# Kernel tuning notes

Measured on AMD Instinct MI355X. Metric: run time of the kernel, lower is better.

The kernel has to match this reference:

```python
import jax, jax.numpy as jnp
import numpy as np

BATCH = 160
INSTANCES = 4
FEAT = 1024
P = BATCH // INSTANCES  # number of identity groups

# sigmas from mmd_loss (original uses float64; fp32 here, tiny sigmas underflow exp to 0 identically)
SIGMAS = np.array([1e-06, 1e-05, 1e-04, 1e-03, 1e-02, 1e-01, 1.0, 5.0, 10.0, 15.0,
                   20.0, 25.0, 30.0, 35.0, 100.0, 1e3, 1e4, 1e5, 1e6], dtype=np.float32)

# replicate the quirky block-pair ordering of the original double loop:
# bct starts with (0,1), then for i in 1..P-1, all j != i.
_PAIRS = [(0, 1)] + [(i, j) for i in range(1, P) for j in range(P) if j != i]
PAIR_I = np.array([p[0] for p in _PAIRS], dtype=np.int32)
PAIR_J = np.array([p[1] for p in _PAIRS], dtype=np.int32)


def _sqdist(a, b):
    # ||a_i - b_j||^2 via matmul identity (same math as euclidean_squared_distance)
    an = jnp.sum(a * a, axis=1)
    bn = jnp.sum(b * b, axis=1)
    return an[:, None] + bn[None, :] - 2.0 * (a @ b.T)


def _gk_mean(x, y):
    # mean over the multi-bandwidth Gaussian kernel matrix: mean(sum_k exp(-d/(2 s_k)))
    d = _sqdist(x, y)
    tot = jnp.float32(0.0)
    for s in SIGMAS:
        tot = tot + jnp.mean(jnp.exp(d * jnp.float32(-1.0 / (2.0 * s))))
    return tot


def _mmd_loss(x, y):
    return _gk_mean(x, x) + _gk_mean(y, y) - 2.0 * _gk_mean(x, y)


def _group_dist_blocks(feats):
    # feats: [BATCH, FEAT] -> all-pairs group distance matrices D[p,q] in [P,P,I,I]
    t = feats.reshape(P, INSTANCES, FEAT)
    tn = jnp.sum(t * t, axis=-1)                      # [P, I]
    cross = jnp.einsum('pif,qjf->pqij', t, t)         # [P, P, I, I]
    D = tn[:, None, :, None] + tn[None, :, None, :] - 2.0 * cross
    wc = D[jnp.arange(P), jnp.arange(P)].reshape(P * INSTANCES, INSTANCES)
    bc = D[PAIR_I, PAIR_J].reshape(-1, INSTANCES)     # [(1+(P-1)^2)*I, I]
    return wc, bc


def setup_inputs() -> dict:
    key = jax.random.key(0)
    k1, k2 = jax.random.split(key)
    return {
        'source_features': jax.random.normal(k1, (BATCH, FEAT), dtype=jnp.float32),
        'target_features': jax.random.normal(k2, (BATCH, FEAT), dtype=jnp.float32),
    }


def reference(source_features, target_features):
    wct, bct = _group_dist_blocks(target_features)
    wcs, bcs = _group_dist_blocks(source_features)
    wcs = jax.lax.stop_gradient(wcs)  # .detach() in original
    bcs = jax.lax.stop_gradient(bcs)
    return (_mmd_loss(wcs, wct), _mmd_loss(bcs, bct))
```

## Files before the change

kernel.cpp:

```cpp
#include <hip/hip_runtime.h>


#define FEAT   1024
#define NROW   160
#define NBC    6088
#define NWC    160
#define NPAD   512

#define WS_ES   0
#define WS_ET   25600
#define WS_BCI  51200
#define WS_WCI  104000
#define WS_TAB  109376
#define WS_ACC_BYTES 460032
#define NSLOT  64

#define TAB_N    2816
#define TAB_BASE 16640

#define GK_BC    6088
#define GK_WCEND 6128
#define GK_GRID  6141

struct Coef { float c[19]; };

#if defined(__has_builtin)
#if __has_builtin(__builtin_amdgcn_exp2f)
#define EXP2(x) __builtin_amdgcn_exp2f(x)
#else
#define EXP2(x) exp2f(x)
#endif
#else
#define EXP2(x) exp2f(x)
#endif

__device__ __forceinline__ float sig13(float d, const Coef& co) {
    float s = 0.f;
    #pragma unroll
    for (int k = 6; k < 19; ++k) s += EXP2(d * co.c[k]);
    return s;
}

__device__ __forceinline__ float sqd(float4 a, float4 b) {
    float d0 = a.x - b.x, d1 = a.y - b.y, d2 = a.z - b.z, d3 = a.w - b.w;
    float d = d0 * d0;
    d = fmaf(d1, d1, d);
    d = fmaf(d2, d2, d);
    return fmaf(d3, d3, d);
}

__global__ __launch_bounds__(256) void compute_E_tab(const float* __restrict__ Fs,
                                                     const float* __restrict__ Ft,
                                                     float* __restrict__ ws, Coef co) {
    int b = blockIdx.x;
    if (b >= 200) {
        int k = (b - 200) * 256 + threadIdx.x;
        unsigned u_lo = (unsigned)(TAB_BASE + k) << 16;
        float d_lo = __uint_as_float(u_lo);
        float d_mi = __uint_as_float(u_lo + 0x8000u);
        float d_hi = __uint_as_float(u_lo + 0x10000u);
        float f_lo = sig13(d_lo, co), f_mi = sig13(d_mi, co), f_hi = sig13(d_hi, co);
        float2 e;
        e.x = f_lo + 0.5f * (f_mi - 0.5f * (f_lo + f_hi));
        e.y = (f_hi - f_lo) * (1.0f / 65536.0f);
        ((float2*)(ws + WS_TAB))[k] = e;
        return;
    }
    int side = b / 100;
    int tile = b % 100;
    int trow = tile / 10, tcol = tile % 10;
    const float* F = side ? Ft : Fs;
    float* E = ws + (side ? WS_ET : WS_ES);

    __shared__ float As[16][132];
    __shared__ float Bs[16][132];
    int tid = threadIdx.x;
    int ti = tid >> 4, tj = tid & 15;
    int lr = tid >> 5;
    int lc4 = tid & 31;

    float acc = 0.f;
    for (int ch = 0; ch < 8; ++ch) {
        for (int rr = lr; rr < 16; rr += 8) {
            float4 a = *(const float4*)(F + (trow*16+rr)*FEAT + ch*128 + lc4*4);
            *(float4*)(&As[rr][lc4*4]) = a;
            float4 bb = *(const float4*)(F + (tcol*16+rr)*FEAT + ch*128 + lc4*4);
            *(float4*)(&Bs[rr][lc4*4]) = bb;
        }
        __syncthreads();
        #pragma unroll
        for (int c = 0; c < 128; c += 4) {
            float4 a = *(const float4*)(&As[ti][c]);
            float4 bb = *(const float4*)(&Bs[tj][c]);
            float d0 = a.x - bb.x, d1 = a.y - bb.y, d2 = a.z - bb.z, d3 = a.w - bb.w;
            acc = fmaf(d0, d0, acc);
            acc = fmaf(d1, d1, acc);
            acc = fmaf(d2, d2, acc);
            acc = fmaf(d3, d3, acc);
        }
        __syncthreads();
    }
    E[(trow*16+ti)*NROW + tcol*16 + tj] = acc;
}

__global__ __launch_bounds__(256) void scatter(float* __restrict__ ws) {
    int idx = blockIdx.x * blockDim.x + threadIdx.x;
    const float* E_s = ws + WS_ES;
    const float* E_t = ws + WS_ET;
    float4* bci = (float4*)(ws + WS_BCI);
    float4* wci = (float4*)(ws + WS_WCI);
    double* accs = (double*)((char*)ws + WS_ACC_BYTES);

    if (idx < 4 * NSLOT) accs[idx] = 0.0;

    if (idx < NBC) {
        int t = idx >> 2, ii = idx & 3;
        int pi, pj;
        if (t == 0) { pi = 0; pj = 1; }
        else {
            int tt = t - 1;
            pi = 1 + tt / 39;
            int jj = tt % 39;
            pj = (jj < pi) ? jj : jj + 1;
        }
        bci[2*idx]   = *(const float4*)(E_s + (4*pi + ii)*NROW + 4*pj);
        bci[2*idx+1] = *(const float4*)(E_t + (4*pi + ii)*NROW + 4*pj);
    } else if (idx < NBC + NWC) {
        int r = idx - NBC;
        int p = r >> 2;
        wci[2*r]   = *(const float4*)(E_s + r*NROW + 4*p);
        wci[2*r+1] = *(const float4*)(E_t + r*NROW + 4*p);
    } else if (idx < NBC + NWC + NPAD) {
        int p = NBC + (idx - (NBC + NWC));
        float4 pad = make_float4(1e19f, 1e19f, 1e19f, 1e19f);
        bci[2*p] = pad;
        bci[2*p+1] = pad;
    } else if (idx < NBC + NWC + 2*NPAD) {
        int p = NWC + (idx - (NBC + NWC + NPAD));
        float4 pad = make_float4(1e19f, 1e19f, 1e19f, 1e19f);
        wci[2*p] = pad;
        wci[2*p+1] = pad;
    }
}

__global__ __launch_bounds__(512, 8) void gk_duo(float* __restrict__ ws) {
    const float4* bci = (const float4*)(ws + WS_BCI);
    const float4* wci = (const float4*)(ws + WS_WCI);
    double* accs = (double*)((char*)ws + WS_ACC_BYTES);

    __shared__ float2 tabs[TAB_N];
    __shared__ float wsum[8][2];

    int tid = threadIdx.x;
    int lane = tid & 63, w = tid >> 6;

    {
        const float4* tg = (const float4*)(ws + WS_TAB);
        float4* td = (float4*)tabs;
        for (int k = tid; k < TAB_N / 2; k += 512) td[k] = tg[k];
    }
    __syncthreads();

    auto tab_get = [&](float d) -> float {
        unsigned u = __float_as_uint(d);
        int t = (int)(u >> 16) - TAB_BASE;
        t = min(max(t, 0), TAB_N - 1);
        float2 e = tabs[t];
        return fmaf((float)(u & 0xFFFFu), e.y, e.x);
    };

    float mc = 0.f, md = 0.f;

    auto duo_sweep = [&](const float4* __restrict__ Yv, int N, int a,
                         int h, int S) {
        float4 xs0 = Yv[2*a],   xt0 = Yv[2*a+1];
        float4 xs1 = Yv[2*a+2], xt1 = Yv[2*a+3];
        if (h == 0 && tid == 0) {
            mc += (tab_get(sqd(xs0, xs1)) + tab_get(sqd(xt0, xt1)))
                - (tab_get(sqd(xs0, xt1)) + tab_get(sqd(xt0, xs1)));
        }
        int jbeg = a + 2;
        int T = (N - jbeg + 511) >> 9;
        int trips = (T - h + S - 1) / S;
        if (trips <= 0) return;
        const float4* Yp = Yv + 2*(jbeg + h*512 + tid);
        int stride = 1024 * S;
        for (int t = 0; t < trips; ++t) {
            float4 ys = Yp[0], yt = Yp[1];
            Yp += stride;
            float a0 = tab_get(sqd(xs0, ys)), a1 = tab_get(sqd(xt0, yt));
            float a2 = tab_get(sqd(xs0, yt)), a3 = tab_get(sqd(xt0, ys));
            float a4 = tab_get(sqd(xs1, ys)), a5 = tab_get(sqd(xt1, yt));
            float a6 = tab_get(sqd(xs1, yt)), a7 = tab_get(sqd(xt1, ys));
            mc += ((a0 + a1) - (a2 + a3)) + ((a4 + a5) - (a6 + a7));
        }
    };

    int b = blockIdx.x;
    int cls;
    if (b < GK_BC) {
        int pp = b >> 2, h = b & 3;
        cls = 1;
        duo_sweep(bci, NBC, 2*pp,        h, 4);
        duo_sweep(bci, NBC, 6086 - 2*pp, h, 4);
    } else if (b < GK_WCEND) {
        int m = b - GK_BC;
        cls = 0;
        duo_sweep(wci, NWC, 2*m,       0, 1);
        duo_sweep(wci, NWC, 158 - 2*m, 0, 1);
    } else {
        int s = b - GK_WCEND;
        if (s < 12) {
            cls = 1;
            int i0 = s * 512 + tid;
            if (i0 < NBC) md += tab_get(sqd(bci[2*i0], bci[2*i0+1]));
        } else {
            cls = 0;
            if (tid < NWC) md += tab_get(sqd(wci[2*tid], wci[2*tid+1]));
        }
    }

    #pragma unroll
    for (int off = 32; off; off >>= 1) {
        mc += __shfl_down(mc, off, 64);
        md += __shfl_down(md, off, 64);
    }
    if (lane == 0) { wsum[w][0] = mc; wsum[w][1] = md; }
    __syncthreads();
    if (tid < 2) {
        double tot = 0.0;
        #pragma unroll
        for (int q = 0; q < 8; ++q) tot += (double)wsum[q][tid];
        if (tot != 0.0)
            atomicAdd(&accs[(cls * 2 + tid) * NSLOT + (b & (NSLOT - 1))], tot);
    }
}

__global__ void finalize(const float* __restrict__ ws, float* __restrict__ out) {
    const double* accs = (const double*)((const char*)ws + WS_ACC_BYTES);
    int lane = threadIdx.x;
    double p[4];
    #pragma unroll
    for (int q = 0; q < 4; ++q) {
        p[q] = accs[q * NSLOT + lane];
        #pragma unroll
        for (int off = 32; off; off >>= 1) p[q] += __shfl_down(p[q], off, 64);
    }
    if (lane == 0) {
        double nw = (double)NWC * (double)NWC;
        double nb = (double)NBC * (double)NBC;
        out[0] = (float)((2.0 * p[0] + 38.0 * NWC - 2.0 * p[1]) / nw);
        out[1] = (float)((2.0 * p[2] + 38.0 * NBC - 2.0 * p[3]) / nb);
    }
}

extern "C" void kernel_launch(void* const* d_in, const int* in_sizes, int n_in,
                              void* d_out, int out_size, void* d_ws, size_t ws_size,
                              hipStream_t stream) {
    const float* src = (const float*)d_in[0];
    const float* tgt = (const float*)d_in[1];
    float* out = (float*)d_out;
    float* ws = (float*)d_ws;

    static const double SIG[19] = {1e-06, 1e-05, 1e-04, 1e-03, 1e-02, 1e-01,
                                   1.0, 5.0, 10.0, 15.0, 20.0, 25.0, 30.0,
                                   35.0, 100.0, 1e3, 1e4, 1e5, 1e6};
    Coef co;
    for (int k = 0; k < 19; ++k)
        co.c[k] = (float)(-1.0 / (2.0 * SIG[k] * 0.6931471805599453));

    compute_E_tab<<<211, 256, 0, stream>>>(src, tgt, ws, co);
    scatter<<<29, 256, 0, stream>>>(ws);
    gk_duo<<<GK_GRID, 512, 0, stream>>>(ws);
    finalize<<<1, 64, 0, stream>>>(ws, out);
}
```

Baseline: 57.44 us.

## Register-block four anchor rows per sweep in pairwise Gaussian kernel pass

The pairwise kernel sweep now holds four anchor rows in registers instead of two, so each loaded partner row is reused across four anchors. The grid shrinks from about 6141 blocks to 1574, with two sweeps per triangle row pair instead of four. Intra-quad pairs get separate blocks. This roughly halves global loads per kernel-table lookup and cuts per-block table-fill overhead, at the cost of more registers and fewer blocks for load balancing.

```diff
diff --git a/kernel.cpp b/kernel.cpp
--- a/kernel.cpp
+++ b/kernel.cpp
@@ -18,9 +18,12 @@
 #define TAB_N    2816
 #define TAB_BASE 16640
 
-#define GK_BC    6088
-#define GK_WCEND 6128
-#define GK_GRID  6141
+#define GK_BCS  1522
+#define GK_WCS  1542
+#define GK_BD   1554
+#define GK_WD   1555
+#define GK_BI   1573
+#define GK_GRID 1574
 
 struct Coef { float c[19]; };
 
@@ -143,7 +146,7 @@
     }
 }
 
-__global__ __launch_bounds__(512, 8) void gk_duo(float* __restrict__ ws) {
+__global__ __launch_bounds__(512, 8) void gk_quad(float* __restrict__ ws) {
     const float4* bci = (const float4*)(ws + WS_BCI);
     const float4* wci = (const float4*)(ws + WS_WCI);
     double* accs = (double*)((char*)ws + WS_ACC_BYTES);
@@ -171,52 +174,70 @@
 
     float mc = 0.f, md = 0.f;
 
-    auto duo_sweep = [&](const float4* __restrict__ Yv, int N, int a,
-                         int h, int S) {
-        float4 xs0 = Yv[2*a],   xt0 = Yv[2*a+1];
-        float4 xs1 = Yv[2*a+2], xt1 = Yv[2*a+3];
-        if (h == 0 && tid == 0) {
-            mc += (tab_get(sqd(xs0, xs1)) + tab_get(sqd(xt0, xt1)))
-                - (tab_get(sqd(xs0, xt1)) + tab_get(sqd(xt0, xs1)));
-        }
-        int jbeg = a + 2;
+    auto combo = [&](float4 xs_, float4 xt_, float4 ys_, float4 yt_) -> float {
+        float d0 = sqd(xs_, ys_), d1 = sqd(xt_, yt_);
+        float d2 = sqd(xs_, yt_), d3 = sqd(xt_, ys_);
+        return (tab_get(d0) + tab_get(d1)) - (tab_get(d2) + tab_get(d3));
+    };
+
+    auto quad_sweep = [&](const float4* __restrict__ Yv, int N, int qa,
+                          int h, int S) {
+        int a = 4 * qa;
+        int jbeg = a + 4;
         int T = (N - jbeg + 511) >> 9;
         int trips = (T - h + S - 1) / S;
         if (trips <= 0) return;
+        float4 xs0 = Yv[2*a],   xt0 = Yv[2*a+1];
+        float4 xs1 = Yv[2*a+2], xt1 = Yv[2*a+3];
+        float4 xs2 = Yv[2*a+4], xt2 = Yv[2*a+5];
+        float4 xs3 = Yv[2*a+6], xt3 = Yv[2*a+7];
         const float4* Yp = Yv + 2*(jbeg + h*512 + tid);
         int stride = 1024 * S;
         for (int t = 0; t < trips; ++t) {
             float4 ys = Yp[0], yt = Yp[1];
             Yp += stride;
-            float a0 = tab_get(sqd(xs0, ys)), a1 = tab_get(sqd(xt0, yt));
-            float a2 = tab_get(sqd(xs0, yt)), a3 = tab_get(sqd(xt0, ys));
-            float a4 = tab_get(sqd(xs1, ys)), a5 = tab_get(sqd(xt1, yt));
-            float a6 = tab_get(sqd(xs1, yt)), a7 = tab_get(sqd(xt1, ys));
-            mc += ((a0 + a1) - (a2 + a3)) + ((a4 + a5) - (a6 + a7));
+            mc += combo(xs0, xt0, ys, yt) + combo(xs1, xt1, ys, yt)
+                + combo(xs2, xt2, ys, yt) + combo(xs3, xt3, ys, yt);
         }
     };
 
     int b = blockIdx.x;
     int cls;
-    if (b < GK_BC) {
-        int pp = b >> 2, h = b & 3;
+    if (b < GK_BCS) {
+        int pp = b >> 1, h = b & 1;
         cls = 1;
-        duo_sweep(bci, NBC, 2*pp,        h, 4);
-        duo_sweep(bci, NBC, 6086 - 2*pp, h, 4);
-    } else if (b < GK_WCEND) {
-        int m = b - GK_BC;
+        quad_sweep(bci, NBC, pp,        h, 2);
+        quad_sweep(bci, NBC, 1521 - pp, h, 2);
+    } else if (b < GK_WCS) {
+        int m = b - GK_BCS;
         cls = 0;
-        duo_sweep(wci, NWC, 2*m,       0, 1);
-        duo_sweep(wci, NWC, 158 - 2*m, 0, 1);
+        quad_sweep(wci, NWC, m,      0, 1);
+        quad_sweep(wci, NWC, 39 - m, 0, 1);
+    } else if (b < GK_BD) {
+        cls = 1;
+        int i0 = (b - GK_WCS) * 512 + tid;
+        if (i0 < NBC) md += tab_get(sqd(bci[2*i0], bci[2*i0+1]));
+    } else if (b < GK_WD) {
+        cls = 0;
+        if (tid < NWC) md += tab_get(sqd(wci[2*tid], wci[2*tid+1]));
+    } else if (b < GK_BI) {
+        cls = 1;
+        int idx = (b - GK_WD) * 512 + tid;
+        if (idx < 1522 * 6) {
+            int q = idx / 6, p = idx % 6;
+            int ao = (p < 3) ? 0 : ((p < 5) ? 1 : 2);
+            int bo = (p < 3) ? (p + 1) : ((p < 5) ? (p - 1) : 3);
+            int i = 4*q + ao, j = 4*q + bo;
+            mc += combo(bci[2*i], bci[2*i+1], bci[2*j], bci[2*j+1]);
+        }
     } else {
-        int s = b - GK_WCEND;
-        if (s < 12) {
-            cls = 1;
-            int i0 = s * 512 + tid;
-            if (i0 < NBC) md += tab_get(sqd(bci[2*i0], bci[2*i0+1]));
-        } else {
-            cls = 0;
-            if (tid < NWC) md += tab_get(sqd(wci[2*tid], wci[2*tid+1]));
+        cls = 0;
+        if (tid < 40 * 6) {
+            int q = tid / 6, p = tid % 6;
+            int ao = (p < 3) ? 0 : ((p < 5) ? 1 : 2);
+            int bo = (p < 3) ? (p + 1) : ((p < 5) ? (p - 1) : 3);
+            int i = 4*q + ao, j = 4*q + bo;
+            mc += combo(wci[2*i], wci[2*i+1], wci[2*j], wci[2*j+1]);
         }
     }
 
@@ -271,6 +292,6 @@
 
     compute_E_tab<<<211, 256, 0, stream>>>(src, tgt, ws, co);
     scatter<<<29, 256, 0, stream>>>(ws);
-    gk_duo<<<GK_GRID, 512, 0, stream>>>(ws);
+    gk_quad<<<GK_GRID, 512, 0, stream>>>(ws);
     finalize<<<1, 64, 0, stream>>>(ws, out);
 }
```

Result: faster. 49.32 us, median of 2 (-14.1%).
